# Performance work log

Hardware: AMD Instinct MI355X
Metric: run time of the kernel (lower is better)

Reference implementation:

```python
import jax, jax.numpy as jnp
import numpy as np

N = 262144      # total nodes
D = 256         # feature channels
B = 1024        # number of graphs (fixed segment count)
EPS = 1e-05


def setup_inputs() -> dict:
    key = jax.random.key(0)
    k1, k2 = jax.random.split(key)
    x = jax.random.normal(k1, (N, D), dtype=jnp.float32)
    batch = jnp.sort(jax.random.randint(k2, (N,), 0, B, dtype=jnp.int64))
    weight = jnp.ones((D,), dtype=jnp.float32)
    bias = jnp.zeros((D,), dtype=jnp.float32)
    return {"x": x, "batch": batch, "weight": weight, "bias": bias}


def reference(x, batch, weight, bias):
    # degree per graph, clamped to >=1, times D (per-graph element count)
    deg = jax.ops.segment_sum(jnp.ones((x.shape[0],), dtype=x.dtype), batch, num_segments=B)
    norm = jnp.clip(deg, 1.0, None)[:, None] * x.shape[-1]          # [B,1]
    # per-graph scalar mean over all nodes and channels
    mean = jax.ops.segment_sum(x, batch, num_segments=B).sum(-1, keepdims=True) / norm  # [B,1]
    xc = x - mean[batch]                                             # [N,D]
    var = jax.ops.segment_sum(xc * xc, batch, num_segments=B).sum(-1, keepdims=True) / norm  # [B,1]
    out = xc / (jnp.sqrt(var)[batch] + EPS)                          # note: eps added after sqrt, as in source
    return out * weight + bias
```

## Files before the change

kernel.cpp:

```cpp
#include <hip/hip_runtime.h>

#define NN 262144
#define DD 256
#define BB 1024
#define GEPS 1e-5f

typedef float floatx4 __attribute__((ext_vector_type(4)));

__global__ __launch_bounds__(512) void k_main(const float4* __restrict__ x,
                                              const int* __restrict__ batch,
                                              const float4* __restrict__ w,
                                              const float4* __restrict__ bi,
                                              float4* __restrict__ out) {
    __shared__ int   s_coarse[2];
    __shared__ int   s_pos[2];
    __shared__ float red_s[8];
    __shared__ float red_q[8];
    __shared__ float bc[2];

    const int b    = blockIdx.x;
    const int tid  = threadIdx.x;
    const int wid  = tid >> 6;
    const int lane = tid & 63;

    if (tid < 2) s_coarse[tid] = NN;
    __syncthreads();
    {
        const int idx = tid << 9;
        const int v   = batch[idx];
        if (v >= b)     atomicMin(&s_coarse[0], idx);
        if (v >= b + 1) atomicMin(&s_coarse[1], idx);
    }
    __syncthreads();
    #pragma unroll
    for (int k = 0; k < 2; ++k) {
        const int tgt = b + k;
        const int cc  = s_coarse[k];
        const int i   = cc - 511 + tid;
        if (i >= 0) {
            const int vi  = (i < NN) ? batch[i] : 0x7fffffff;
            const int vim = (i > 0) ? batch[i - 1] : (-2147483647 - 1);
            if (vi >= tgt && vim < tgt) s_pos[k] = i;
        }
    }
    __syncthreads();
    const int s0 = s_pos[0];
    const int s1 = s_pos[1];
    if (s1 <= s0) return;

    float s = 0.0f, q = 0.0f;
    for (int r = s0 + wid; r < s1; r += 8) {
        float4 v = x[r * 64 + lane];
        s += v.x + v.y + v.z + v.w;
        q += v.x * v.x + v.y * v.y + v.z * v.z + v.w * v.w;
    }
    #pragma unroll
    for (int off = 32; off; off >>= 1) {
        s += __shfl_down(s, off, 64);
        q += __shfl_down(q, off, 64);
    }
    if (lane == 0) { red_s[wid] = s; red_q[wid] = q; }
    __syncthreads();
    if (tid == 0) {
        float ts = 0.0f, tq = 0.0f;
        #pragma unroll
        for (int i = 0; i < 8; ++i) { ts += red_s[i]; tq += red_q[i]; }
        const float norm = (float)(s1 - s0) * (float)DD;
        const float mean = ts / norm;
        const float var  = fmaxf(tq / norm - mean * mean, 0.0f);
        bc[0] = mean;
        bc[1] = 1.0f / (sqrtf(var) + GEPS);
    }
    __syncthreads();
    const float  mean = bc[0];
    const float  inv  = bc[1];
    const float4 wv   = w[lane];
    const float4 bv   = bi[lane];

    for (int r = s0 + wid; r < s1; r += 8) {
        float4 v = x[r * 64 + lane];
        floatx4 o;
        o.x = (v.x - mean) * inv * wv.x + bv.x;
        o.y = (v.y - mean) * inv * wv.y + bv.y;
        o.z = (v.z - mean) * inv * wv.z + bv.z;
        o.w = (v.w - mean) * inv * wv.w + bv.w;
        __builtin_nontemporal_store(o, (floatx4*)&out[r * 64 + lane]);
    }
}

extern "C" void kernel_launch(void* const* d_in, const int* in_sizes, int n_in,
                              void* d_out, int out_size, void* d_ws, size_t ws_size,
                              hipStream_t stream) {
    const float4* x     = (const float4*)d_in[0];
    const int*    batch = (const int*)d_in[1];
    const float4* w     = (const float4*)d_in[2];
    const float4* bi    = (const float4*)d_in[3];
    float4*       out   = (float4*)d_out;

    k_main<<<BB, 512, 0, stream>>>(x, batch, w, bi, out);
}
```

Before: 130.9 us.

## Cache segment rows in registers between stats and normalize passes

The first pass now loads up to 32 rows per wave into a register array and the second pass normalizes from registers instead of reading x from global memory again. Rows past that limit fall back to a second global read. This targets the doubled HBM read traffic of the two-pass scheme. In exchange it uses about 128 extra VGPRs per thread (launch bounds set to 2 blocks of 512), which lowers occupancy and could cause spills, and it serializes loads behind per-row predicates.

New measurement: 133.9 us. 2.3% more time.

```diff
diff --git a/kernel.cpp b/kernel.cpp
--- a/kernel.cpp
+++ b/kernel.cpp
@@ -4,14 +4,15 @@
 #define DD 256
 #define BB 1024
 #define GEPS 1e-5f
+#define NCHUNK 32
 
 typedef float floatx4 __attribute__((ext_vector_type(4)));
 
-__global__ __launch_bounds__(512) void k_main(const float4* __restrict__ x,
-                                              const int* __restrict__ batch,
-                                              const float4* __restrict__ w,
-                                              const float4* __restrict__ bi,
-                                              float4* __restrict__ out) {
+__global__ __launch_bounds__(512, 2) void k_main(const float4* __restrict__ x,
+                                                 const int* __restrict__ batch,
+                                                 const float4* __restrict__ w,
+                                                 const float4* __restrict__ bi,
+                                                 float4* __restrict__ out) {
     __shared__ int   s_coarse[2];
     __shared__ int   s_pos[2];
     __shared__ float red_s[8];
@@ -49,11 +50,24 @@
     if (s1 <= s0) return;
 
     float s = 0.0f, q = 0.0f;
-    for (int r = s0 + wid; r < s1; r += 8) {
-        float4 v = x[r * 64 + lane];
-        s += v.x + v.y + v.z + v.w;
-        q += v.x * v.x + v.y * v.y + v.z * v.z + v.w * v.w;
+    float4 v[NCHUNK];
+    const int rbase = s0 + wid;
+    #pragma unroll
+    for (int i = 0; i < NCHUNK; ++i) {
+        const int r = rbase + i * 8;
+        if (r < s1) {
+            const float4 t4 = x[r * 64 + lane];
+            v[i] = t4;
+            s += t4.x + t4.y + t4.z + t4.w;
+            q += t4.x * t4.x + t4.y * t4.y + t4.z * t4.z + t4.w * t4.w;
+        }
     }
+    for (int r = rbase + NCHUNK * 8; r < s1; r += 8) {
+        const float4 t4 = x[r * 64 + lane];
+        s += t4.x + t4.y + t4.z + t4.w;
+        q += t4.x * t4.x + t4.y * t4.y + t4.z * t4.z + t4.w * t4.w;
+    }
+
     #pragma unroll
     for (int off = 32; off; off >>= 1) {
         s += __shfl_down(s, off, 64);
@@ -77,13 +91,25 @@
     const float4 wv   = w[lane];
     const float4 bv   = bi[lane];
 
-    for (int r = s0 + wid; r < s1; r += 8) {
-        float4 v = x[r * 64 + lane];
+    #pragma unroll
+    for (int i = 0; i < NCHUNK; ++i) {
+        const int r = rbase + i * 8;
+        if (r < s1) {
+            floatx4 o;
+            o.x = (v[i].x - mean) * inv * wv.x + bv.x;
+            o.y = (v[i].y - mean) * inv * wv.y + bv.y;
+            o.z = (v[i].z - mean) * inv * wv.z + bv.z;
+            o.w = (v[i].w - mean) * inv * wv.w + bv.w;
+            __builtin_nontemporal_store(o, (floatx4*)&out[r * 64 + lane]);
+        }
+    }
+    for (int r = rbase + NCHUNK * 8; r < s1; r += 8) {
+        const float4 t4 = x[r * 64 + lane];
         floatx4 o;
-        o.x = (v.x - mean) * inv * wv.x + bv.x;
-        o.y = (v.y - mean) * inv * wv.y + bv.y;
-        o.z = (v.z - mean) * inv * wv.z + bv.z;
-        o.w = (v.w - mean) * inv * wv.w + bv.w;
+        o.x = (t4.x - mean) * inv * wv.x + bv.x;
+        o.y = (t4.y - mean) * inv * wv.y + bv.y;
+        o.z = (t4.z - mean) * inv * wv.z + bv.z;
+        o.w = (t4.w - mean) * inv * wv.w + bv.w;
         __builtin_nontemporal_store(o, (floatx4*)&out[r * 64 + lane]);
     }
 }
```
